# Performance work log

Hardware: AMD Instinct MI355X
Metric: run time of the kernel (lower is better)

## Reference

```python
import jax, jax.numpy as jnp
import numpy as np

N = 100000        # nodes
E = 1600000       # edges (avg degree 16)
D = 128           # feature dim (in_dim == out_dim)
L = 3             # num_layers
P = 8             # num_parts


def setup_inputs() -> dict:
    key = jax.random.key(0)
    k1, k2, k3, k4, k5, k6 = jax.random.split(key, 6)
    edge_row = jnp.sort(jax.random.randint(k1, (E,), 0, N))
    edge_col = jax.random.randint(k2, (E,), 0, N)
    edge_vals = jax.random.uniform(k3, (E,), dtype=jnp.float32)
    x = jax.random.normal(k4, (N, D), dtype=jnp.float32)
    stacked_params = jax.random.normal(k5, (L, D, D, P), dtype=jnp.float32)
    layer_weights = jax.random.normal(k6, (L, P), dtype=jnp.float32)
    return {"edge_row": edge_row, "edge_col": edge_col, "edge_vals": edge_vals,
            "x": x, "stacked_params": stacked_params, "layer_weights": layer_weights}


def reference(edge_row, edge_col, edge_vals, x, stacked_params, layer_weights):
    n = x.shape[0]
    num_layers = stacked_params.shape[0]
    h = x
    for i in range(num_layers):
        # sparse adj.spmm(h): gather source features, scale by edge value, sum per row
        msg = h[edge_col] * edge_vals[:, None]                       # [E, D]
        ax = jax.ops.segment_sum(msg, edge_row, num_segments=n)      # [N, D]
        # MyLinear: softmax over the num_parts weight, contract parts dim
        w = jax.nn.softmax(layer_weights[i])                         # [P]
        ww = jnp.einsum('oip,p->oi', stacked_params[i], w)           # [D_out, D_in]
        h = ax @ ww.T                                                # [N, D_out]
        if i < num_layers - 1:
            h = jax.nn.relu(h)
    return h
```

## Files before the change

### kernel.cpp

```cpp
#include <hip/hip_runtime.h>
#include <cstdint>

#define D 128
#define P 8
#define L 3

typedef __attribute__((ext_vector_type(8))) _Float16 f16x8;
typedef __attribute__((ext_vector_type(4))) float    f32x4;
typedef __attribute__((ext_vector_type(2))) float    f32x2;

#if __has_builtin(__builtin_amdgcn_cvt_pk_f32_fp8) && __has_builtin(__builtin_amdgcn_cvt_pk_fp8_f32)
#define HAVE_FP8_CVT 1
#else
#define HAVE_FP8_CVT 0
#endif

template<bool HI>
static __device__ __forceinline__ f32x2 fp8_pair(uint32_t u) {
#if HAVE_FP8_CVT
    return __builtin_amdgcn_cvt_pk_f32_fp8((int)u, HI);
#else
    uint32_t w = HI ? (u >> 16) : u;
    f32x2 r;
#pragma unroll
    for (int i = 0; i < 2; i++) {
        uint32_t b = (w >> (8 * i)) & 0xffu;
        uint32_t mag = b & 0x7fu;
        uint16_t h = (uint16_t)(((b & 0x80u) << 8) | ((mag >= 8u) ? ((mag << 7) + 0x2000u) : 0u));
        union { uint16_t q; _Float16 hf; } c; c.q = h;
        r[i] = (float)c.hf;
    }
    return r;
#endif
}

static __device__ __forceinline__ uint32_t f32_to_fp8(float v) {
#if HAVE_FP8_CVT
    return (uint32_t)__builtin_amdgcn_cvt_pk_fp8_f32(v, v, 0, false) & 0xffu;
#else
    union { _Float16 hf; uint16_t q; } c; c.hf = (_Float16)v;
    uint32_t s = ((uint32_t)c.q >> 8) & 0x80u;
    int t = (int)(c.q & 0x7fff) - 0x2000;
    if (t < 0) return s;
    int r = (t + 63 + ((t >> 7) & 1)) >> 7;
    if (r > 0x7e) r = 0x7e;
    return s | (uint32_t)r;
#endif
}

__global__ void prep_edges(const int* __restrict__ er, const int* __restrict__ col,
                           const float* __restrict__ vals,
                           int* __restrict__ rp, uint32_t* __restrict__ epk,
                           int n, int e) {
    int i = blockIdx.x * blockDim.x + threadIdx.x;
    if (i >= e) return;
    union { _Float16 h; uint16_t u; } v;
    v.h = (_Float16)vals[i];
    epk[i] = ((uint32_t)col[i] << 15) | (uint32_t)(v.u & 0x7FFFu);

    int cur = er[i];
    if (i == 0) {
        for (int r = 0; r <= cur; r++) rp[r] = 0;
    } else {
        int prev = er[i - 1];
        for (int r = prev + 1; r <= cur; r++) rp[r] = i;
    }
    if (i == e - 1) {
        for (int r = cur + 1; r <= n; r++) rp[r] = e;
    }
}

__global__ void build_ww(const float* __restrict__ sp, const float* __restrict__ lw,
                         _Float16* __restrict__ wwB) {
    int idx = blockIdx.x * blockDim.x + threadIdx.x;
    if (idx >= L * D * D) return;
    int l = idx / (D * D);
    int rem = idx - l * D * D;
    int o = rem / D;
    int i = rem - o * D;
    float wv[P];
    float m = -1e30f;
#pragma unroll
    for (int p = 0; p < P; p++) { wv[p] = lw[l * P + p]; m = fmaxf(m, wv[p]); }
    float s = 0.f;
#pragma unroll
    for (int p = 0; p < P; p++) { wv[p] = __expf(wv[p] - m); s += wv[p]; }
    float inv = 1.0f / s;
    const float* spp = sp + ((size_t)(l * D + o) * D + i) * P;
    float acc = 0.f;
#pragma unroll
    for (int p = 0; p < P; p++) acc += spp[p] * wv[p];
    int kt = i >> 5, kp = i & 31;
    wwB[(((l * 4 + kt) * D + o) << 5) + kp] = (_Float16)(acc * inv);
}

static __device__ __forceinline__ void mfma_store16_q8(const _Float16 (*s_h)[136],
                                                       const _Float16* __restrict__ wwB_l,
                                                       uint8_t* __restrict__ y8,
                                                       float* __restrict__ scl,
                                                       unsigned* srow,
                                                       int row0, int n, int tid) {
    const int w = tid >> 6, lane = tid & 63;
    const int quad = lane >> 4, l16 = lane & 15;
    f32x4 acc[2] = {};
#pragma unroll
    for (int kt = 0; kt < 4; kt++) {
        f16x8 af = *(const f16x8*)&s_h[l16][kt * 32 + quad * 8];
#pragma unroll
        for (int c = 0; c < 2; c++) {
            const int ct = w * 2 + c;
            f16x8 bf = *(const f16x8*)&wwB_l[((kt * D + ct * 16 + l16) << 5) + quad * 8];
            acc[c] = __builtin_amdgcn_mfma_f32_16x16x32_f16(af, bf, acc[c], 0, 0, 0);
        }
    }
#pragma unroll
    for (int rg = 0; rg < 4; rg++) {
        float m = fmaxf(fabsf(acc[0][rg]), fabsf(acc[1][rg]));
#pragma unroll
        for (int d = 1; d < 16; d <<= 1) m = fmaxf(m, __shfl_xor(m, d));
        if (l16 == 0) atomicMax(&srow[quad * 4 + rg], __float_as_uint(m));
    }
    __syncthreads();
#pragma unroll
    for (int rg = 0; rg < 4; rg++) {
        const int rr = quad * 4 + rg;
        const int row = row0 + rr;
        float rmax = fmaxf(__uint_as_float(srow[rr]), 1e-20f);
        float qs = 448.f / rmax;
        if (row < n) {
#pragma unroll
            for (int c = 0; c < 2; c++) {
                const int ct = w * 2 + c;
                float v = acc[c][rg] * qs;
                v = fminf(fmaxf(v, -448.f), 448.f);
                y8[row * D + ct * 16 + l16] = (uint8_t)f32_to_fp8(v);
            }
            if (w == 0 && l16 == 0) scl[row] = rmax * (1.f / 448.f);
        }
    }
}

__global__ __launch_bounds__(256, 8)
void gemm_x32(const float* __restrict__ x, const _Float16* __restrict__ wwB_l,
              uint8_t* __restrict__ y8, float* __restrict__ scl, int n) {
    __shared__ _Float16 s_h[16][136];
    __shared__ unsigned srow[16];
    const int tid = threadIdx.x;
    const int row0 = blockIdx.x * 16;
    const int c8 = (tid & 15) * 8;
    if (tid < 16) srow[tid] = 0;
    {
        int r = tid >> 4;
        int row = row0 + r;
        float4 v0 = {}, v1 = {};
        if (row < n) {
            v0 = *(const float4*)&x[row * D + c8];
            v1 = *(const float4*)&x[row * D + c8 + 4];
        }
        f16x8 h;
        h[0] = (_Float16)v0.x; h[1] = (_Float16)v0.y;
        h[2] = (_Float16)v0.z; h[3] = (_Float16)v0.w;
        h[4] = (_Float16)v1.x; h[5] = (_Float16)v1.y;
        h[6] = (_Float16)v1.z; h[7] = (_Float16)v1.w;
        *(f16x8*)&s_h[r][c8] = h;
    }
    __syncthreads();
    mfma_store16_q8(s_h, wwB_l, y8, scl, srow, row0, n, tid);
}

template<int NB>
static __device__ __forceinline__ void gather_chunk8(float (&a)[8],
                                                     const uint8_t* __restrict__ y8,
                                                     const uint32_t* __restrict__ epk,
                                                     const float* __restrict__ scl,
                                                     int e, int c8) {
    uint32_t m[NB];
#pragma unroll
    for (int j = 0; j < NB; j++) m[j] = epk[e + j];
    uint2 g[NB]; float sc[NB];
#pragma unroll
    for (int j = 0; j < NB; j++) {
        uint32_t row = m[j] >> 15;
        g[j]  = *(const uint2*)&y8[row * (uint32_t)D + (uint32_t)c8];
        sc[j] = scl[row];
    }
#pragma unroll
    for (int j = 0; j < NB; j++) {
        union { uint16_t u; _Float16 h; } vv; vv.u = (uint16_t)(m[j] & 0x7FFFu);
        float vf = (float)vv.h * sc[j];
        f32x2 p;
        p = fp8_pair<false>(g[j].x); a[0] += vf * p[0]; a[1] += vf * p[1];
        p = fp8_pair<true >(g[j].x); a[2] += vf * p[0]; a[3] += vf * p[1];
        p = fp8_pair<false>(g[j].y); a[4] += vf * p[0]; a[5] += vf * p[1];
        p = fp8_pair<true >(g[j].y); a[6] += vf * p[0]; a[7] += vf * p[1];
    }
}

static __device__ __forceinline__ void gather_row8(float (&a)[8],
                                                   const uint8_t* __restrict__ y8,
                                                   const uint32_t* __restrict__ epk,
                                                   const float* __restrict__ scl,
                                                   int e, int e1, int c8) {
    for (; e + 8 <= e1; e += 8) gather_chunk8<8>(a, y8, epk, scl, e, c8);
    if (e + 4 <= e1) { gather_chunk8<4>(a, y8, epk, scl, e, c8); e += 4; }
    for (; e < e1; e++) gather_chunk8<1>(a, y8, epk, scl, e, c8);
}

__global__ __launch_bounds__(256, 6)
void fused_layer(const uint8_t* __restrict__ yprev, const float* __restrict__ sprev,
                 const int* __restrict__ rp, const uint32_t* __restrict__ epk,
                 const _Float16* __restrict__ wwB_l,
                 uint8_t* __restrict__ ynext, float* __restrict__ snext, int n) {
    __shared__ _Float16 s_h[16][136];
    __shared__ unsigned srow[16];
    const int tid = threadIdx.x;
    const int row0 = blockIdx.x * 16;
    const int sg = tid >> 4;
    const int c8 = (tid & 15) * 8;
    if (tid < 16) srow[tid] = 0;
    {
        int r = row0 + sg;
        float a[8] = {0.f, 0.f, 0.f, 0.f, 0.f, 0.f, 0.f, 0.f};
        if (r < n) gather_row8(a, yprev, epk, sprev, rp[r], rp[r + 1], c8);
        f16x8 o;
#pragma unroll
        for (int k = 0; k < 8; k++) o[k] = (_Float16)fmaxf(a[k], 0.f);
        *(f16x8*)&s_h[sg][c8] = o;
    }
    __syncthreads();
    mfma_store16_q8(s_h, wwB_l, ynext, snext, srow, row0, n, tid);
}

__global__ __launch_bounds__(256, 6)
void spmm_f32(const uint8_t* __restrict__ y8, const float* __restrict__ sprev,
              const int* __restrict__ rp, const uint32_t* __restrict__ epk,
              float* __restrict__ out, int n) {
    const int tid = threadIdx.x;
    const int r = blockIdx.x * 16 + (tid >> 4);
    const int c8 = (tid & 15) * 8;
    if (r >= n) return;
    float a[8] = {0.f, 0.f, 0.f, 0.f, 0.f, 0.f, 0.f, 0.f};
    gather_row8(a, y8, epk, sprev, rp[r], rp[r + 1], c8);
    *(float4*)&out[(size_t)r * D + c8]     = make_float4(a[0], a[1], a[2], a[3]);
    *(float4*)&out[(size_t)r * D + c8 + 4] = make_float4(a[4], a[5], a[6], a[7]);
}

extern "C" void kernel_launch(void* const* d_in, const int* in_sizes, int n_in,
                              void* d_out, int out_size, void* d_ws, size_t ws_size,
                              hipStream_t stream) {
    const int*   edge_row  = (const int*)d_in[0];
    const int*   edge_col  = (const int*)d_in[1];
    const float* edge_vals = (const float*)d_in[2];
    const float* x         = (const float*)d_in[3];
    const float* sp        = (const float*)d_in[4];
    const float* lw        = (const float*)d_in[5];
    float* out = (float*)d_out;

    const int E_ = in_sizes[0];
    const int N_ = in_sizes[3] / D;

    char* ws = (char*)d_ws;
    int* row_ptr = (int*)ws;
    size_t off = (((size_t)(N_ + 1) * sizeof(int)) + 255) & ~(size_t)255;
    uint32_t* epk = (uint32_t*)(ws + off);
    off += (size_t)E_ * sizeof(uint32_t);
    off = (off + 255) & ~(size_t)255;
    _Float16* wwB = (_Float16*)(ws + off);
    off += (size_t)L * 4 * D * 32 * sizeof(_Float16);
    off = (off + 255) & ~(size_t)255;
    uint8_t* y8A = (uint8_t*)(ws + off);
    off += (size_t)N_ * D;
    uint8_t* y8B = (uint8_t*)(ws + off);
    off += (size_t)N_ * D;
    off = (off + 255) & ~(size_t)255;
    float* scA = (float*)(ws + off);
    off += (size_t)N_ * sizeof(float);
    float* scB = (float*)(ws + off);

    prep_edges<<<(E_ + 255) / 256, 256, 0, stream>>>(edge_row, edge_col, edge_vals,
                                                     row_ptr, epk, N_, E_);
    build_ww<<<(L * D * D + 255) / 256, 256, 0, stream>>>(sp, lw, wwB);

    const int sblk = (N_ + 15) / 16;
    const int WWL = 4 * D * 32;

    gemm_x32<<<sblk, 256, 0, stream>>>(x, wwB, y8A, scA, N_);
    fused_layer<<<sblk, 256, 0, stream>>>(y8A, scA, row_ptr, epk, wwB + WWL,     y8B, scB, N_);
    fused_layer<<<sblk, 256, 0, stream>>>(y8B, scB, row_ptr, epk, wwB + 2 * WWL, y8A, scA, N_);
    spmm_f32<<<sblk, 256, 0, stream>>>(y8A, scA, row_ptr, epk, out, N_);
}
```

Before: 266.7 us.

## Merge prep kernels, halve block size, and software-pipeline edge index loads in gather

```diff
diff --git a/kernel.cpp b/kernel.cpp
--- a/kernel.cpp
+++ b/kernel.cpp
@@ -8,6 +8,8 @@
 typedef __attribute__((ext_vector_type(8))) _Float16 f16x8;
 typedef __attribute__((ext_vector_type(4))) float    f32x4;
 typedef __attribute__((ext_vector_type(2))) float    f32x2;
+typedef __attribute__((ext_vector_type(4))) uint32_t u32x4;
+typedef u32x4 __attribute__((aligned(4))) u32x4_u;
 
 #if __has_builtin(__builtin_amdgcn_cvt_pk_f32_fp8) && __has_builtin(__builtin_amdgcn_cvt_pk_fp8_f32)
 #define HAVE_FP8_CVT 1
@@ -48,74 +50,72 @@
 #endif
 }
 
-__global__ void prep_edges(const int* __restrict__ er, const int* __restrict__ col,
-                           const float* __restrict__ vals,
-                           int* __restrict__ rp, uint32_t* __restrict__ epk,
-                           int n, int e) {
+__global__ void prep_all(const int* __restrict__ er, const int* __restrict__ col,
+                         const float* __restrict__ vals,
+                         const float* __restrict__ sp, const float* __restrict__ lw,
+                         int* __restrict__ rp, uint32_t* __restrict__ epk,
+                         _Float16* __restrict__ wwB, int n, int e) {
     int i = blockIdx.x * blockDim.x + threadIdx.x;
-    if (i >= e) return;
-    union { _Float16 h; uint16_t u; } v;
-    v.h = (_Float16)vals[i];
-    epk[i] = ((uint32_t)col[i] << 15) | (uint32_t)(v.u & 0x7FFFu);
-
-    int cur = er[i];
-    if (i == 0) {
-        for (int r = 0; r <= cur; r++) rp[r] = 0;
-    } else {
-        int prev = er[i - 1];
-        for (int r = prev + 1; r <= cur; r++) rp[r] = i;
-    }
-    if (i == e - 1) {
-        for (int r = cur + 1; r <= n; r++) rp[r] = e;
-    }
-}
-
-__global__ void build_ww(const float* __restrict__ sp, const float* __restrict__ lw,
-                         _Float16* __restrict__ wwB) {
-    int idx = blockIdx.x * blockDim.x + threadIdx.x;
-    if (idx >= L * D * D) return;
-    int l = idx / (D * D);
-    int rem = idx - l * D * D;
-    int o = rem / D;
-    int i = rem - o * D;
-    float wv[P];
-    float m = -1e30f;
-#pragma unroll
-    for (int p = 0; p < P; p++) { wv[p] = lw[l * P + p]; m = fmaxf(m, wv[p]); }
-    float s = 0.f;
-#pragma unroll
-    for (int p = 0; p < P; p++) { wv[p] = __expf(wv[p] - m); s += wv[p]; }
-    float inv = 1.0f / s;
-    const float* spp = sp + ((size_t)(l * D + o) * D + i) * P;
-    float acc = 0.f;
-#pragma unroll
-    for (int p = 0; p < P; p++) acc += spp[p] * wv[p];
-    int kt = i >> 5, kp = i & 31;
-    wwB[(((l * 4 + kt) * D + o) << 5) + kp] = (_Float16)(acc * inv);
-}
-
-static __device__ __forceinline__ void mfma_store16_q8(const _Float16 (*s_h)[136],
-                                                       const _Float16* __restrict__ wwB_l,
-                                                       uint8_t* __restrict__ y8,
-                                                       float* __restrict__ scl,
-                                                       unsigned* srow,
-                                                       int row0, int n, int tid) {
+    if (i < e) {
+        union { _Float16 h; uint16_t u; } v;
+        v.h = (_Float16)vals[i];
+        epk[i] = ((uint32_t)col[i] << 15) | (uint32_t)(v.u & 0x7FFFu);
+        int cur = er[i];
+        if (i == 0) {
+            for (int r = 0; r <= cur; r++) rp[r] = 0;
+        } else {
+            int prev = er[i - 1];
+            for (int r = prev + 1; r <= cur; r++) rp[r] = i;
+        }
+        if (i == e - 1) {
+            for (int r = cur + 1; r <= n; r++) rp[r] = e;
+        }
+    }
+    if (i < L * D * D) {
+        int l = i / (D * D);
+        int rem = i - l * D * D;
+        int o = rem / D;
+        int ii = rem - o * D;
+        float wv[P];
+        float m = -1e30f;
+#pragma unroll
+        for (int p = 0; p < P; p++) { wv[p] = lw[l * P + p]; m = fmaxf(m, wv[p]); }
+        float s = 0.f;
+#pragma unroll
+        for (int p = 0; p < P; p++) { wv[p] = __expf(wv[p] - m); s += wv[p]; }
+        float inv = 1.0f / s;
+        const float* spp = sp + ((size_t)(l * D + o) * D + ii) * P;
+        float acc = 0.f;
+#pragma unroll
+        for (int p = 0; p < P; p++) acc += spp[p] * wv[p];
+        int kt = ii >> 5, kp = ii & 31;
+        wwB[(((l * 4 + kt) * D + o) << 5) + kp] = (_Float16)(acc * inv);
+    }
+}
+
+static __device__ __forceinline__ void mfma2w_q8(const _Float16 (*s_h)[136],
+                                                 const _Float16* __restrict__ wwB_l,
+                                                 uint8_t* __restrict__ y8,
+                                                 float* __restrict__ scl,
+                                                 unsigned* srow,
+                                                 int row0, int n, int tid) {
     const int w = tid >> 6, lane = tid & 63;
     const int quad = lane >> 4, l16 = lane & 15;
-    f32x4 acc[2] = {};
+    f32x4 acc[4] = {};
 #pragma unroll
     for (int kt = 0; kt < 4; kt++) {
         f16x8 af = *(const f16x8*)&s_h[l16][kt * 32 + quad * 8];
 #pragma unroll
-        for (int c = 0; c < 2; c++) {
-            const int ct = w * 2 + c;
+        for (int c = 0; c < 4; c++) {
+            const int ct = w * 4 + c;
             f16x8 bf = *(const f16x8*)&wwB_l[((kt * D + ct * 16 + l16) << 5) + quad * 8];
             acc[c] = __builtin_amdgcn_mfma_f32_16x16x32_f16(af, bf, acc[c], 0, 0, 0);
         }
     }
 #pragma unroll
     for (int rg = 0; rg < 4; rg++) {
-        float m = fmaxf(fabsf(acc[0][rg]), fabsf(acc[1][rg]));
+        float m = fmaxf(fmaxf(fabsf(acc[0][rg]), fabsf(acc[1][rg])),
+                        fmaxf(fabsf(acc[2][rg]), fabsf(acc[3][rg])));
 #pragma unroll
         for (int d = 1; d < 16; d <<= 1) m = fmaxf(m, __shfl_xor(m, d));
         if (l16 == 0) atomicMax(&srow[quad * 4 + rg], __float_as_uint(m));
@@ -129,8 +129,8 @@
         float qs = 448.f / rmax;
         if (row < n) {
 #pragma unroll
-            for (int c = 0; c < 2; c++) {
-                const int ct = w * 2 + c;
+            for (int c = 0; c < 4; c++) {
+                const int ct = w * 4 + c;
                 float v = acc[c][rg] * qs;
                 v = fminf(fmaxf(v, -448.f), 448.f);
                 y8[row * D + ct * 16 + l16] = (uint8_t)f32_to_fp8(v);
@@ -140,18 +140,20 @@
     }
 }
 
-__global__ __launch_bounds__(256, 8)
+__global__ __launch_bounds__(128, 8)
 void gemm_x32(const float* __restrict__ x, const _Float16* __restrict__ wwB_l,
               uint8_t* __restrict__ y8, float* __restrict__ scl, int n) {
     __shared__ _Float16 s_h[16][136];
     __shared__ unsigned srow[16];
     const int tid = threadIdx.x;
     const int row0 = blockIdx.x * 16;
+    const int sg = tid >> 4;
     const int c8 = (tid & 15) * 8;
     if (tid < 16) srow[tid] = 0;
-    {
-        int r = tid >> 4;
-        int row = row0 + r;
+#pragma unroll
+    for (int h2 = 0; h2 < 2; h2++) {
+        int rr = sg + h2 * 8;
+        int row = row0 + rr;
         float4 v0 = {}, v1 = {};
         if (row < n) {
             v0 = *(const float4*)&x[row * D + c8];
@@ -162,10 +164,10 @@
         h[2] = (_Float16)v0.z; h[3] = (_Float16)v0.w;
         h[4] = (_Float16)v1.x; h[5] = (_Float16)v1.y;
         h[6] = (_Float16)v1.z; h[7] = (_Float16)v1.w;
-        *(f16x8*)&s_h[r][c8] = h;
+        *(f16x8*)&s_h[rr][c8] = h;
     }
     __syncthreads();
-    mfma_store16_q8(s_h, wwB_l, y8, scl, srow, row0, n, tid);
+    mfma2w_q8(s_h, wwB_l, y8, scl, srow, row0, n, tid);
 }
 
 template<int NB>
@@ -196,17 +198,48 @@
     }
 }
 
-static __device__ __forceinline__ void gather_row8(float (&a)[8],
-                                                   const uint8_t* __restrict__ y8,
-                                                   const uint32_t* __restrict__ epk,
-                                                   const float* __restrict__ scl,
-                                                   int e, int e1, int c8) {
-    for (; e + 8 <= e1; e += 8) gather_chunk8<8>(a, y8, epk, scl, e, c8);
+static __device__ __forceinline__ void gather_row8_pipe(float (&a)[8],
+                                                        const uint8_t* __restrict__ y8,
+                                                        const uint32_t* __restrict__ epk,
+                                                        const float* __restrict__ scl,
+                                                        int e, int e1, int c8) {
+    const int nfull = (e1 - e) >> 3;
+    u32x4 mA = {}, mB = {};
+    if (nfull > 0) {
+        mA = *(const u32x4_u*)&epk[e];
+        mB = *(const u32x4_u*)&epk[e + 4];
+    }
+    for (int c = 0; c < nfull; c++) {
+        uint32_t m[8] = { mA.x, mA.y, mA.z, mA.w, mB.x, mB.y, mB.z, mB.w };
+        uint2 g[8]; float sc[8];
+#pragma unroll
+        for (int j = 0; j < 8; j++) {
+            uint32_t row = m[j] >> 15;
+            g[j]  = *(const uint2*)&y8[row * (uint32_t)D + (uint32_t)c8];
+            sc[j] = scl[row];
+        }
+        if (c + 1 < nfull) {
+            const int en = e + (c + 1) * 8;
+            mA = *(const u32x4_u*)&epk[en];
+            mB = *(const u32x4_u*)&epk[en + 4];
+        }
+#pragma unroll
+        for (int j = 0; j < 8; j++) {
+            union { uint16_t u; _Float16 h; } vv; vv.u = (uint16_t)(m[j] & 0x7FFFu);
+            float vf = (float)vv.h * sc[j];
+            f32x2 p;
+            p = fp8_pair<false>(g[j].x); a[0] += vf * p[0]; a[1] += vf * p[1];
+            p = fp8_pair<true >(g[j].x); a[2] += vf * p[0]; a[3] += vf * p[1];
+            p = fp8_pair<false>(g[j].y); a[4] += vf * p[0]; a[5] += vf * p[1];
+            p = fp8_pair<true >(g[j].y); a[6] += vf * p[0]; a[7] += vf * p[1];
+        }
+    }
+    e += nfull * 8;
     if (e + 4 <= e1) { gather_chunk8<4>(a, y8, epk, scl, e, c8); e += 4; }
     for (; e < e1; e++) gather_chunk8<1>(a, y8, epk, scl, e, c8);
 }
 
-__global__ __launch_bounds__(256, 6)
+__global__ __launch_bounds__(128, 8)
 void fused_layer(const uint8_t* __restrict__ yprev, const float* __restrict__ sprev,
                  const int* __restrict__ rp, const uint32_t* __restrict__ epk,
                  const _Float16* __restrict__ wwB_l,
@@ -218,29 +251,31 @@
     const int sg = tid >> 4;
     const int c8 = (tid & 15) * 8;
     if (tid < 16) srow[tid] = 0;
-    {
-        int r = row0 + sg;
+#pragma unroll
+    for (int h2 = 0; h2 < 2; h2++) {
+        const int rr = sg + h2 * 8;
+        const int r = row0 + rr;
         float a[8] = {0.f, 0.f, 0.f, 0.f, 0.f, 0.f, 0.f, 0.f};
-        if (r < n) gather_row8(a, yprev, epk, sprev, rp[r], rp[r + 1], c8);
+        if (r < n) gather_row8_pipe(a, yprev, epk, sprev, rp[r], rp[r + 1], c8);
         f16x8 o;
 #pragma unroll
         for (int k = 0; k < 8; k++) o[k] = (_Float16)fmaxf(a[k], 0.f);
-        *(f16x8*)&s_h[sg][c8] = o;
+        *(f16x8*)&s_h[rr][c8] = o;
     }
     __syncthreads();
-    mfma_store16_q8(s_h, wwB_l, ynext, snext, srow, row0, n, tid);
-}
-
-__global__ __launch_bounds__(256, 6)
+    mfma2w_q8(s_h, wwB_l, ynext, snext, srow, row0, n, tid);
+}
+
+__global__ __launch_bounds__(128, 8)
 void spmm_f32(const uint8_t* __restrict__ y8, const float* __restrict__ sprev,
               const int* __restrict__ rp, const uint32_t* __restrict__ epk,
               float* __restrict__ out, int n) {
     const int tid = threadIdx.x;
-    const int r = blockIdx.x * 16 + (tid >> 4);
+    const int r = blockIdx.x * 8 + (tid >> 4);
     const int c8 = (tid & 15) * 8;
     if (r >= n) return;
     float a[8] = {0.f, 0.f, 0.f, 0.f, 0.f, 0.f, 0.f, 0.f};
-    gather_row8(a, y8, epk, sprev, rp[r], rp[r + 1], c8);
+    gather_row8_pipe(a, y8, epk, sprev, rp[r], rp[r + 1], c8);
     *(float4*)&out[(size_t)r * D + c8]     = make_float4(a[0], a[1], a[2], a[3]);
     *(float4*)&out[(size_t)r * D + c8 + 4] = make_float4(a[4], a[5], a[6], a[7]);
 }
@@ -277,15 +312,15 @@
     off += (size_t)N_ * sizeof(float);
     float* scB = (float*)(ws + off);
 
-    prep_edges<<<(E_ + 255) / 256, 256, 0, stream>>>(edge_row, edge_col, edge_vals,
-                                                     row_ptr, epk, N_, E_);
-    build_ww<<<(L * D * D + 255) / 256, 256, 0, stream>>>(sp, lw, wwB);
+    const int pgrid = (E_ > L * D * D ? E_ : L * D * D);
+    prep_all<<<(pgrid + 255) / 256, 256, 0, stream>>>(edge_row, edge_col, edge_vals,
+                                                      sp, lw, row_ptr, epk, wwB, N_, E_);
 
     const int sblk = (N_ + 15) / 16;
     const int WWL = 4 * D * 32;
 
-    gemm_x32<<<sblk, 256, 0, stream>>>(x, wwB, y8A, scA, N_);
-    fused_layer<<<sblk, 256, 0, stream>>>(y8A, scA, row_ptr, epk, wwB + WWL,     y8B, scB, N_);
-    fused_layer<<<sblk, 256, 0, stream>>>(y8B, scB, row_ptr, epk, wwB + 2 * WWL, y8A, scA, N_);
-    spmm_f32<<<sblk, 256, 0, stream>>>(y8A, scA, row_ptr, epk, out, N_);
-}
+    gemm_x32<<<sblk, 128, 0, stream>>>(x, wwB, y8A, scA, N_);
+    fused_layer<<<sblk, 128, 0, stream>>>(y8A, scA, row_ptr, epk, wwB + WWL,     y8B, scB, N_);
+    fused_layer<<<sblk, 128, 0, stream>>>(y8B, scB, row_ptr, epk, wwB + 2 * WWL, y8A, scA, N_);
+    spmm_f32<<<(N_ + 7) / 8, 128, 0, stream>>>(y8A, scA, row_ptr, epk, out, N_);
+}
```

After: 270.9 us. About the same (+1.6%).
